# Kernel tuning notes

Measured on AMD Instinct MI355X. Metric: run time of the kernel, lower is better.

Reference implementation:

```python
import jax, jax.numpy as jnp
import numpy as np

IN_DIM = 32
OUT_DIM = 32
VAR_DIM = 64
BATCH = 16384
KER_DIMS = [1024, 1024, 1024, 1024]
NUM_STEPS = 8  # fixed-step RK4 stand-in for adaptive odeint (tol=1e-4)


def setup_inputs() -> dict:
    key = jax.random.key(0)
    ks = jax.random.split(key, 12)
    x = jax.random.normal(ks[0], (BATCH, IN_DIM), dtype=jnp.float32)
    aug = jnp.ones((BATCH, VAR_DIM - IN_DIM), dtype=jnp.float32)
    dims = [VAR_DIM] + KER_DIMS + [VAR_DIM]
    inp = {"x": x, "aug": aug}
    for i, (d1, d2) in enumerate(zip(dims[:-1], dims[1:])):
        # Linear(d1+1, d2): weight (d2, d1+1), bias (d2,)
        inp[f"W{i}"] = jax.random.normal(ks[1 + 2 * i], (d2, d1 + 1), dtype=jnp.float32) * 0.02
        inp[f"b{i}"] = jax.random.normal(ks[2 + 2 * i], (d2,), dtype=jnp.float32) * 0.02
    return inp


def _odefunc(t, y, Ws, bs):
    # y: [B, VAR_DIM]; per-layer concat of scalar time column, Linear, ReLU (except last)
    out = y
    n = len(Ws)
    for i, (W, b) in enumerate(zip(Ws, bs)):
        z = jnp.concatenate([out, jnp.full((out.shape[0], 1), t, dtype=out.dtype)], axis=1)
        out = z @ W.T + b
        if i < n - 1:
            out = jax.nn.relu(out)
    return out


def _integrate(y0, Ws, bs):
    dt = jnp.float32(1.0 / NUM_STEPS)

    def rk4_step(y, t):
        k1 = _odefunc(t, y, Ws, bs)
        k2 = _odefunc(t + 0.5 * dt, y + 0.5 * dt * k1, Ws, bs)
        k3 = _odefunc(t + 0.5 * dt, y + 0.5 * dt * k2, Ws, bs)
        k4 = _odefunc(t + dt, y + dt * k3, Ws, bs)
        return y + (dt / 6.0) * (k1 + 2.0 * k2 + 2.0 * k3 + k4), None

    ts = jnp.arange(NUM_STEPS, dtype=jnp.float32) * dt
    y1, _ = jax.lax.scan(rk4_step, y0, ts)
    return y1


def reference(x, aug, W0, b0, W1, b1, W2, b2, W3, b3, W4, b4):
    Ws = (W0, W1, W2, W3, W4)
    bs = (b0, b1, b2, b3, b4)
    y0 = jnp.concatenate([x, aug], axis=1)  # [B, VAR_DIM]
    y1 = _integrate(y0, Ws, bs)
    return y1[:, :OUT_DIM]
```

## Files before the change

kernel.cpp:

```cpp
#include <hip/hip_runtime.h>
#include <cstdint>
#include <cstddef>

#define BATCH 16384

typedef float f32x4 __attribute__((ext_vector_type(4)));
typedef _Float16 f16x8 __attribute__((ext_vector_type(8)));

__device__ __forceinline__ unsigned short f2h_bits(float f) {
  _Float16 h = (_Float16)f;
  return __builtin_bit_cast(unsigned short, h);
}

__device__ __forceinline__ void async_cp16(const void* g, void* l) {
  __builtin_amdgcn_global_load_lds(
      (const __attribute__((address_space(1))) unsigned int*)g,
      (__attribute__((address_space(3))) unsigned int*)l, 16, 0, 0);
}

#define PIPE_BAR_3() asm volatile("s_waitcnt vmcnt(3)\n\ts_barrier" ::: "memory")
#define PIPE_BAR_0() asm volatile("s_waitcnt vmcnt(0)\n\ts_barrier" ::: "memory")

template <int BM, int BN, int RT, int CT, int K, int N, bool RELU>
__launch_bounds__(512, 4)
__global__ void gemm_h(const unsigned short* __restrict__ A,
                       const unsigned short* __restrict__ Bw,
                       const float* __restrict__ Wfull,
                       const float* __restrict__ bias,
                       float tval,
                       unsigned short* __restrict__ Ch) {
  constexpr int BK = 32;
  constexpr int NI = K / BK;
  static_assert(NI >= 2, "pipeline needs >=2 stages");
  static_assert((BM * 4 + BN * 4) / 512 == 3, "vmcnt(3) assumes 3 loads/stage");
  static_assert(BM == 4 * RT * 16 && BN == 2 * CT * 16, "4x2 waves");
  __shared__ __align__(16) unsigned short smA[3][BM * BK];
  __shared__ __align__(16) unsigned short smB[3][BN * BK];
  __shared__ float biasLds[BN];

  const int tid = threadIdx.x;
  const int wave = tid >> 6;
  const int lane = tid & 63;
  const int quad = lane >> 4;
  const int r16 = lane & 15;

  const int rowA0 = blockIdx.x * BM;
  const int rowB0 = blockIdx.y * BN;
  const int waveM = wave >> 1;
  const int waveN = wave & 1;

  if (tid < BN) {
    const int col = rowB0 + tid;
    biasLds[tid] = bias[col] + tval * Wfull[(size_t)col * (K + 1) + K];
  }

  auto stage = [&](int k0, int buf) {
#pragma unroll
    for (int i = 0; i < BM * 4 / 512; ++i) {
      const int s = i * 512 + tid;
      const int row = s >> 2;
      const int c = (s & 3) ^ ((row >> 1) & 3);
      const unsigned short* g = A + (size_t)(rowA0 + row) * K + (k0 + c * 8);
      char* l = ((char*)smA[buf]) + (size_t)(i * 512 + (wave << 6)) * 16;
      async_cp16(g, l);
    }
    {
      const int s = tid;
      const int row = s >> 2;
      const int c = (s & 3) ^ ((row >> 1) & 3);
      const unsigned short* g = Bw + (size_t)(rowB0 + row) * K + (k0 + c * 8);
      char* l = ((char*)smB[buf]) + (size_t)((wave << 6)) * 16;
      async_cp16(g, l);
    }
  };

  f32x4 acc[RT][CT];
  const f32x4 zero = {0.f, 0.f, 0.f, 0.f};
#pragma unroll
  for (int i = 0; i < RT; ++i)
#pragma unroll
    for (int j = 0; j < CT; ++j) acc[i][j] = zero;

  auto compute = [&](int buf) {
    const unsigned short* sA = smA[buf];
    const unsigned short* sB = smB[buf];
    f16x8 af[RT], bfr[CT];
#pragma unroll
    for (int nt = 0; nt < CT; ++nt) {
      const int row = waveN * (CT * 16) + nt * 16 + r16;
      const int cp = quad ^ ((row >> 1) & 3);
      bfr[nt] = *(const f16x8*)(sB + row * BK + cp * 8);
    }
#pragma unroll
    for (int mt = 0; mt < RT; ++mt) {
      const int row = waveM * (RT * 16) + mt * 16 + r16;
      const int cp = quad ^ ((row >> 1) & 3);
      af[mt] = *(const f16x8*)(sA + row * BK + cp * 8);
    }
#pragma unroll
    for (int mt = 0; mt < RT; ++mt)
#pragma unroll
      for (int nt = 0; nt < CT; ++nt)
        acc[mt][nt] =
            __builtin_amdgcn_mfma_f32_16x16x32_f16(af[mt], bfr[nt], acc[mt][nt], 0, 0, 0);
  };

  stage(0, 0);
  stage(BK, 1);

#pragma unroll
  for (int kk = 0; kk < NI - 1; ++kk) {
    PIPE_BAR_3();
    if (kk + 2 < NI) stage((kk + 2) * BK, (kk + 2) % 3);
    compute(kk % 3);
  }
  PIPE_BAR_0();
  compute((NI - 1) % 3);

#pragma unroll
  for (int mt = 0; mt < RT; ++mt) {
    const int grow0 = rowA0 + waveM * (RT * 16) + mt * 16 + quad * 4;
#pragma unroll
    for (int nt = 0; nt < CT; ++nt) {
      const int lcol = waveN * (CT * 16) + nt * 16 + r16;
      const int gcol = rowB0 + lcol;
      const float bi = biasLds[lcol];
#pragma unroll
      for (int r = 0; r < 4; ++r) {
        float v = acc[mt][nt][r] + bi;
        if (RELU) v = fmaxf(v, 0.0f);
        Ch[(size_t)(grow0 + r) * N + gcol] = f2h_bits(v);
      }
    }
  }
}

__launch_bounds__(256, 4)
__global__ void gemm_l4(const unsigned short* __restrict__ A,
                        const unsigned short* __restrict__ Bw,
                        const float* __restrict__ Wfull,
                        const float* __restrict__ bias,
                        float tval,
                        float* __restrict__ y, float* __restrict__ ksum,
                        unsigned short* __restrict__ yh,
                        float* __restrict__ outp, int mode, float dt) {
  constexpr int K = 1024, BK = 32, BM = 32, BN = 64, NI = K / BK;
  __shared__ __align__(16) unsigned short smA[2][BM * BK];
  __shared__ __align__(16) unsigned short smB[2][BN * BK];
  __shared__ float biasLds[BN];

  const int tid = threadIdx.x;
  const int wave = tid >> 6;
  const int lane = tid & 63;
  const int quad = lane >> 4;
  const int r16 = lane & 15;

  const int rowA0 = blockIdx.x * BM;
  const int waveM = wave >> 1;
  const int waveN = wave & 1;

  if (tid < BN) {
    biasLds[tid] = bias[tid] + tval * Wfull[(size_t)tid * (K + 1) + K];
  }

  auto stage = [&](int k0, int buf) {
    if (tid < BM * 4) {
      const int s = tid;
      const int row = s >> 2;
      const int c = (s & 3) ^ ((row >> 1) & 3);
      const unsigned short* g = A + (size_t)(rowA0 + row) * K + (k0 + c * 8);
      char* l = ((char*)smA[buf]) + (size_t)(wave << 6) * 16;
      async_cp16(g, l);
    }
    {
      const int s = tid;
      const int row = s >> 2;
      const int c = (s & 3) ^ ((row >> 1) & 3);
      const unsigned short* g = Bw + (size_t)row * K + (k0 + c * 8);
      char* l = ((char*)smB[buf]) + (size_t)(wave << 6) * 16;
      async_cp16(g, l);
    }
  };

  f32x4 acc[2];
  const f32x4 zero = {0.f, 0.f, 0.f, 0.f};
  acc[0] = zero; acc[1] = zero;

  stage(0, 0);

#pragma unroll 2
  for (int kk = 0; kk < NI; ++kk) {
    __syncthreads();
    if (kk + 1 < NI) stage((kk + 1) * BK, (kk + 1) & 1);

    const unsigned short* sA = smA[kk & 1];
    const unsigned short* sB = smB[kk & 1];
    f16x8 af, bfr[2];
    {
      const int row = waveM * 16 + r16;
      const int cp = quad ^ ((row >> 1) & 3);
      af = *(const f16x8*)(sA + row * BK + cp * 8);
    }
#pragma unroll
    for (int nt = 0; nt < 2; ++nt) {
      const int row = (waveN * 2 + nt) * 16 + r16;
      const int cp = quad ^ ((row >> 1) & 3);
      bfr[nt] = *(const f16x8*)(sB + row * BK + cp * 8);
    }
#pragma unroll
    for (int nt = 0; nt < 2; ++nt)
      acc[nt] = __builtin_amdgcn_mfma_f32_16x16x32_f16(af, bfr[nt], acc[nt], 0, 0, 0);
  }

  const int grow0 = rowA0 + waveM * 16 + quad * 4;
#pragma unroll
  for (int nt = 0; nt < 2; ++nt) {
    const int col = waveN * 32 + nt * 16 + r16;
    const float bi = biasLds[col];
#pragma unroll
    for (int r = 0; r < 4; ++r) {
      const float k = acc[nt][r] + bi;
      const int row = grow0 + r;
      const int idx = row * 64 + col;
      if (mode == 0) {
        ksum[idx] = k;
        yh[idx] = f2h_bits(y[idx] + 0.5f * dt * k);
      } else if (mode == 1) {
        ksum[idx] += 2.f * k;
        yh[idx] = f2h_bits(y[idx] + 0.5f * dt * k);
      } else if (mode == 2) {
        ksum[idx] += 2.f * k;
        yh[idx] = f2h_bits(y[idx] + dt * k);
      } else {
        const float yn = y[idx] + (dt / 6.f) * (ksum[idx] + k);
        y[idx] = yn;
        yh[idx] = f2h_bits(yn);
        if (outp && col < 32) outp[row * 32 + col] = yn;
      }
    }
  }
}

__global__ void conv_w(const float* __restrict__ W, unsigned short* __restrict__ Wh,
                       int N, int K) {
  const int idx = blockIdx.x * 256 + threadIdx.x;
  if (idx < N * K) {
    const int n = idx / K;
    const int k = idx - n * K;
    Wh[idx] = f2h_bits(W[(size_t)n * (K + 1) + k]);
  }
}

__global__ void init_y(const float* __restrict__ x, const float* __restrict__ aug,
                       float* __restrict__ y, unsigned short* __restrict__ yh) {
  const int idx = blockIdx.x * 256 + threadIdx.x;
  const int i = idx >> 6;
  const int j = idx & 63;
  const float v = (j < 32) ? x[i * 32 + j] : aug[i * 32 + (j - 32)];
  y[idx] = v;
  yh[idx] = f2h_bits(v);
}

extern "C" void kernel_launch(void* const* d_in, const int* in_sizes, int n_in,
                              void* d_out, int out_size, void* d_ws, size_t ws_size,
                              hipStream_t stream) {
  const float* x = (const float*)d_in[0];
  const float* aug = (const float*)d_in[1];
  const float* W[5];
  const float* b[5];
  for (int i = 0; i < 5; ++i) {
    W[i] = (const float*)d_in[2 + 2 * i];
    b[i] = (const float*)d_in[3 + 2 * i];
  }

  char* ws = (char*)d_ws;
  auto alloc = [&](size_t bytes) -> char* {
    char* p = ws;
    ws += (bytes + 255) & ~(size_t)255;
    return p;
  };
  float* y = (float*)alloc((size_t)BATCH * 64 * 4);
  unsigned short* yh = (unsigned short*)alloc((size_t)BATCH * 64 * 2);
  unsigned short* h1 = (unsigned short*)alloc((size_t)BATCH * 1024 * 2);
  unsigned short* h2 = (unsigned short*)alloc((size_t)BATCH * 1024 * 2);
  float* ksum = (float*)alloc((size_t)BATCH * 64 * 4);
  const int Kdim[5] = {64, 1024, 1024, 1024, 1024};
  const int Ndim[5] = {1024, 1024, 1024, 1024, 64};
  unsigned short* Wh[5];
  for (int i = 0; i < 5; ++i)
    Wh[i] = (unsigned short*)alloc((size_t)Ndim[i] * Kdim[i] * 2);

  for (int i = 0; i < 5; ++i) {
    const int total = Ndim[i] * Kdim[i];
    conv_w<<<(total + 255) / 256, 256, 0, stream>>>(W[i], Wh[i], Ndim[i], Kdim[i]);
  }
  init_y<<<BATCH * 64 / 256, 256, 0, stream>>>(x, aug, y, yh);

  const float dt = 0.125f;
  float* outp = (float*)d_out;

  auto eval = [&](float t, int mode, float* op) {
    gemm_h<256, 128, 4, 4, 64, 1024, true>
        <<<dim3(BATCH / 256, 1024 / 128), 512, 0, stream>>>(
            yh, Wh[0], W[0], b[0], t, h1);
    unsigned short* src = h1;
    unsigned short* dst = h2;
    for (int L = 1; L <= 3; ++L) {
      gemm_h<256, 128, 4, 4, 1024, 1024, true>
          <<<dim3(BATCH / 256, 1024 / 128), 512, 0, stream>>>(
              src, Wh[L], W[L], b[L], t, dst);
      unsigned short* tmp = src; src = dst; dst = tmp;
    }
    gemm_l4<<<dim3(BATCH / 32, 1), 256, 0, stream>>>(
        src, Wh[4], W[4], b[4], t, y, ksum, yh, op, mode, dt);
  };

  for (int s = 0; s < 8; ++s) {
    const float t0 = s * dt;
    eval(t0, 0, nullptr);
    eval(t0 + 0.5f * dt, 1, nullptr);
    eval(t0 + 0.5f * dt, 2, nullptr);
    eval(t0 + dt, 3, (s == 7) ? outp : nullptr);
  }
}
```

Measured before the change: 4.499 ms.

## Add 256x256 pipelined GEMM kernel with phased LDS loads for hidden layers

Replaces the 256x128 tile GEMM used for the three 1024x1024 hidden layers with a new 256x256 tile kernel using BK=64, double-buffered async global-to-LDS staging split across four phases per tile, XOR-swizzled LDS, and setprio around the MFMA bursts. The larger tile raises arithmetic intensity per loaded byte, and interleaving staging with compute is meant to hide global load latency. It uses 128 KB of LDS and many accumulator registers, which limits occupancy, and the grid shrinks to 256 blocks.

```diff
diff --git a/kernel.cpp b/kernel.cpp
--- a/kernel.cpp
+++ b/kernel.cpp
@@ -130,6 +130,142 @@
         float v = acc[mt][nt][r] + bi;
         if (RELU) v = fmaxf(v, 0.0f);
         Ch[(size_t)(grow0 + r) * N + gcol] = f2h_bits(v);
+      }
+    }
+  }
+}
+
+#define SBAR  asm volatile("s_barrier" ::: "memory")
+#define MBAR  asm volatile("s_waitcnt lgkmcnt(0)\n\ts_barrier" ::: "memory")
+#define VBAR8 asm volatile("s_waitcnt vmcnt(8)\n\ts_barrier" ::: "memory")
+#define VBAR0 asm volatile("s_waitcnt vmcnt(0)\n\ts_barrier" ::: "memory")
+
+#define PHASE(sA_, sB_, Q, STAGE_STMT, BND)                                   \
+  {                                                                           \
+    if ((Q) == 0) {                                                           \
+      _Pragma("unroll") for (int nt = 0; nt < 4; ++nt) {                      \
+        const int row = wc * 64 + nt * 16 + r16;                              \
+        const int sw = row & 7;                                               \
+        const unsigned short* bp = (sB_) + row * 64;                          \
+        bfr[nt][0] = *(const f16x8*)(bp + ((quad ^ sw) << 3));                \
+        bfr[nt][1] = *(const f16x8*)(bp + (((4 + quad) ^ sw) << 3));          \
+      }                                                                       \
+    }                                                                         \
+    f16x8 af0[2], af1[2];                                                     \
+    _Pragma("unroll") for (int mi = 0; mi < 2; ++mi) {                        \
+      const int row = wr * 128 + ((Q) * 2 + mi) * 16 + r16;                   \
+      const int sw = row & 7;                                                 \
+      const unsigned short* ap = (sA_) + row * 64;                            \
+      af0[mi] = *(const f16x8*)(ap + ((quad ^ sw) << 3));                     \
+      af1[mi] = *(const f16x8*)(ap + (((4 + quad) ^ sw) << 3));               \
+    }                                                                         \
+    MBAR;                                                                     \
+    STAGE_STMT;                                                               \
+    __builtin_amdgcn_s_setprio(1);                                            \
+    _Pragma("unroll") for (int mi = 0; mi < 2; ++mi)                          \
+      _Pragma("unroll") for (int nt = 0; nt < 4; ++nt) {                      \
+        acc[(Q) * 2 + mi][nt] = __builtin_amdgcn_mfma_f32_16x16x32_f16(       \
+            af0[mi], bfr[nt][0], acc[(Q) * 2 + mi][nt], 0, 0, 0);             \
+        acc[(Q) * 2 + mi][nt] = __builtin_amdgcn_mfma_f32_16x16x32_f16(       \
+            af1[mi], bfr[nt][1], acc[(Q) * 2 + mi][nt], 0, 0, 0);             \
+      }                                                                       \
+    __builtin_amdgcn_s_setprio(0);                                            \
+    BND;                                                                      \
+  }
+
+#define TILE(sA_, sB_, STG0, STG1, STG3, BND)  \
+  {                                            \
+    f16x8 bfr[4][2];                           \
+    PHASE(sA_, sB_, 0, STG0, SBAR)             \
+    PHASE(sA_, sB_, 1, STG1, SBAR)             \
+    PHASE(sA_, sB_, 2, ;, SBAR)                \
+    PHASE(sA_, sB_, 3, STG3, BND)              \
+  }
+
+__launch_bounds__(512, 2)
+__global__ void gemm8(const unsigned short* __restrict__ A,
+                      const unsigned short* __restrict__ Bw,
+                      const float* __restrict__ Wfull,
+                      const float* __restrict__ bias,
+                      float tval,
+                      unsigned short* __restrict__ Ch) {
+  __shared__ __align__(16) unsigned short smA[2][256 * 64];
+  __shared__ __align__(16) unsigned short smB[2][256 * 64];
+  __shared__ float biasLds[256];
+
+  const int tid = threadIdx.x;
+  const int wave = tid >> 6;
+  const int lane = tid & 63;
+  const int quad = lane >> 4;
+  const int r16 = lane & 15;
+  const int wr = wave >> 2;
+  const int wc = wave & 3;
+
+  const int rowA0 = blockIdx.x * 256;
+  const int rowB0 = blockIdx.y * 256;
+  const unsigned short* Ag = A + (size_t)rowA0 * 1024;
+  const unsigned short* Bg = Bw + (size_t)rowB0 * 1024;
+
+  if (tid < 256) {
+    const int col = rowB0 + tid;
+    biasLds[tid] = bias[col] + tval * Wfull[(size_t)col * 1025 + 1024];
+  }
+
+  auto stg = [&](const unsigned short* gbase, unsigned short* lds, int k0, int half) {
+#pragma unroll
+    for (int i = 0; i < 2; ++i) {
+      const int s = half * 1024 + i * 512 + tid;
+      const int row = s >> 3;
+      const int c = (s & 7) ^ (row & 7);
+      const unsigned short* g = gbase + (size_t)row * 1024 + (k0 + (c << 3));
+      char* l = (char*)lds + (size_t)(half * 1024 + i * 512 + (wave << 6)) * 16;
+      async_cp16(g, l);
+    }
+  };
+
+  f32x4 acc[8][4];
+  const f32x4 zero = {0.f, 0.f, 0.f, 0.f};
+#pragma unroll
+  for (int i = 0; i < 8; ++i)
+#pragma unroll
+    for (int j = 0; j < 4; ++j) acc[i][j] = zero;
+
+  stg(Bg, smB[0], 0, 0);  stg(Bg, smB[0], 0, 1);
+  stg(Ag, smA[0], 0, 0);  stg(Ag, smA[0], 0, 1);
+  stg(Bg, smB[1], 64, 0); stg(Bg, smB[1], 64, 1);
+  stg(Ag, smA[1], 64, 0); stg(Ag, smA[1], 64, 1);
+  VBAR8;
+
+  for (int tt = 0; tt < 14; tt += 2) {
+    const int kn0 = (tt + 2) * 64;
+    const int kn1 = (tt + 3) * 64;
+    TILE(smA[0], smB[0],
+         stg(Bg, smB[0], kn0, 0),
+         stg(Bg, smB[0], kn0, 1),
+         (stg(Ag, smA[0], kn0, 0), stg(Ag, smA[0], kn0, 1)),
+         VBAR8)
+    TILE(smA[1], smB[1],
+         stg(Bg, smB[1], kn1, 0),
+         stg(Bg, smB[1], kn1, 1),
+         (stg(Ag, smA[1], kn1, 0), stg(Ag, smA[1], kn1, 1)),
+         VBAR8)
+  }
+  TILE(smA[0], smB[0], ;, ;, ;, VBAR0)
+  TILE(smA[1], smB[1], ;, ;, ;, ;)
+
+#pragma unroll
+  for (int mt = 0; mt < 8; ++mt) {
+    const int grow0 = rowA0 + wr * 128 + mt * 16 + quad * 4;
+#pragma unroll
+    for (int nt = 0; nt < 4; ++nt) {
+      const int lcol = wc * 64 + nt * 16 + r16;
+      const int gcol = rowB0 + lcol;
+      const float bi = biasLds[lcol];
+#pragma unroll
+      for (int r = 0; r < 4; ++r) {
+        float v = acc[mt][nt][r] + bi;
+        v = fmaxf(v, 0.0f);
+        Ch[(size_t)(grow0 + r) * 1024 + gcol] = f2h_bits(v);
       }
     }
   }
@@ -306,9 +442,8 @@
     unsigned short* src = h1;
     unsigned short* dst = h2;
     for (int L = 1; L <= 3; ++L) {
-      gemm_h<256, 128, 4, 4, 1024, 1024, true>
-          <<<dim3(BATCH / 256, 1024 / 128), 512, 0, stream>>>(
-              src, Wh[L], W[L], b[L], t, dst);
+      gemm8<<<dim3(BATCH / 256, 1024 / 256), 512, 0, stream>>>(
+          src, Wh[L], W[L], b[L], t, dst);
       unsigned short* tmp = src; src = dst; dst = tmp;
     }
     gemm_l4<<<dim3(BATCH / 32, 1), 256, 0, stream>>>(
```

After: 4.473 ms. About the same (-0.6%).

## Load hidden-layer weight fragments directly from global, staging only activations in LDS

Applied to the files above, without the earlier changes.

Adds a gemm_hb variant for the three 1024x1024 hidden layers. Only the activation tile goes through the async global-to-LDS triple buffer. Each wave reads its weight (B) fragments straight from global memory into registers every K step, and the pipeline wait is lowered to vmcnt(2). This cuts LDS traffic and shared-memory footprint and drops the B staging loads, but it exposes global/L2 load latency on the B fragments inside each iteration. Those fragments are also loaded redundantly by the four waves that share a column slice.

```diff
diff --git a/kernel.cpp b/kernel.cpp
--- a/kernel.cpp
+++ b/kernel.cpp
@@ -19,6 +19,7 @@
 }
 
 #define PIPE_BAR_3() asm volatile("s_waitcnt vmcnt(3)\n\ts_barrier" ::: "memory")
+#define PIPE_BAR_2() asm volatile("s_waitcnt vmcnt(2)\n\ts_barrier" ::: "memory")
 #define PIPE_BAR_0() asm volatile("s_waitcnt vmcnt(0)\n\ts_barrier" ::: "memory")
 
 template <int BM, int BN, int RT, int CT, int K, int N, bool RELU>
@@ -116,6 +117,109 @@
   }
   PIPE_BAR_0();
   compute((NI - 1) % 3);
+
+#pragma unroll
+  for (int mt = 0; mt < RT; ++mt) {
+    const int grow0 = rowA0 + waveM * (RT * 16) + mt * 16 + quad * 4;
+#pragma unroll
+    for (int nt = 0; nt < CT; ++nt) {
+      const int lcol = waveN * (CT * 16) + nt * 16 + r16;
+      const int gcol = rowB0 + lcol;
+      const float bi = biasLds[lcol];
+#pragma unroll
+      for (int r = 0; r < 4; ++r) {
+        float v = acc[mt][nt][r] + bi;
+        if (RELU) v = fmaxf(v, 0.0f);
+        Ch[(size_t)(grow0 + r) * N + gcol] = f2h_bits(v);
+      }
+    }
+  }
+}
+
+template <int BM, int BN, int RT, int CT, int K, int N, bool RELU>
+__launch_bounds__(512, 4)
+__global__ void gemm_hb(const unsigned short* __restrict__ A,
+                        const unsigned short* __restrict__ Bw,
+                        const float* __restrict__ Wfull,
+                        const float* __restrict__ bias,
+                        float tval,
+                        unsigned short* __restrict__ Ch) {
+  constexpr int BK = 32;
+  constexpr int NI = K / BK;
+  static_assert(NI >= 2, "pipeline needs >=2 stages");
+  static_assert(BM * 4 / 512 == 2, "A stage = 2 loads/thread");
+  static_assert(BM == 4 * RT * 16 && BN == 2 * CT * 16, "4x2 waves");
+  __shared__ __align__(16) unsigned short smA[3][BM * BK];
+  __shared__ float biasLds[BN];
+
+  const int tid = threadIdx.x;
+  const int wave = tid >> 6;
+  const int lane = tid & 63;
+  const int quad = lane >> 4;
+  const int r16 = lane & 15;
+
+  const int rowA0 = blockIdx.x * BM;
+  const int rowB0 = blockIdx.y * BN;
+  const int waveM = wave >> 1;
+  const int waveN = wave & 1;
+
+  if (tid < BN) {
+    const int col = rowB0 + tid;
+    biasLds[tid] = bias[col] + tval * Wfull[(size_t)col * (K + 1) + K];
+  }
+
+  auto stage = [&](int k0, int buf) {
+#pragma unroll
+    for (int i = 0; i < 2; ++i) {
+      const int s = i * 512 + tid;
+      const int row = s >> 2;
+      const int c = (s & 3) ^ ((row >> 1) & 3);
+      const unsigned short* g = A + (size_t)(rowA0 + row) * K + (k0 + c * 8);
+      char* l = ((char*)smA[buf]) + (size_t)(i * 512 + (wave << 6)) * 16;
+      async_cp16(g, l);
+    }
+  };
+
+  f32x4 acc[RT][CT];
+  const f32x4 zero = {0.f, 0.f, 0.f, 0.f};
+#pragma unroll
+  for (int i = 0; i < RT; ++i)
+#pragma unroll
+    for (int j = 0; j < CT; ++j) acc[i][j] = zero;
+
+  stage(0, 0);
+  stage(BK, 1);
+
+#pragma unroll
+  for (int kk = 0; kk < NI; ++kk) {
+    PIPE_BAR_2();
+
+    f16x8 bfr[CT];
+#pragma unroll
+    for (int nt = 0; nt < CT; ++nt) {
+      const int row = rowB0 + waveN * (CT * 16) + nt * 16 + r16;
+      bfr[nt] = *(const f16x8*)(Bw + (size_t)row * K + kk * BK + quad * 8);
+    }
+    __builtin_amdgcn_sched_barrier(0);
+
+    if (kk + 2 < NI) stage((kk + 2) * BK, (kk + 2) % 3);
+    __builtin_amdgcn_sched_barrier(0);
+
+    const unsigned short* sA = smA[kk % 3];
+    f16x8 af[RT];
+#pragma unroll
+    for (int mt = 0; mt < RT; ++mt) {
+      const int row = waveM * (RT * 16) + mt * 16 + r16;
+      const int cp = quad ^ ((row >> 1) & 3);
+      af[mt] = *(const f16x8*)(sA + row * BK + cp * 8);
+    }
+#pragma unroll
+    for (int mt = 0; mt < RT; ++mt)
+#pragma unroll
+      for (int nt = 0; nt < CT; ++nt)
+        acc[mt][nt] =
+            __builtin_amdgcn_mfma_f32_16x16x32_f16(af[mt], bfr[nt], acc[mt][nt], 0, 0, 0);
+  }
 
 #pragma unroll
   for (int mt = 0; mt < RT; ++mt) {
@@ -306,7 +410,7 @@
     unsigned short* src = h1;
     unsigned short* dst = h2;
     for (int L = 1; L <= 3; ++L) {
-      gemm_h<256, 128, 4, 4, 1024, 1024, true>
+      gemm_hb<256, 128, 4, 4, 1024, 1024, true>
           <<<dim3(BATCH / 256, 1024 / 128), 512, 0, stream>>>(
               src, Wh[L], W[L], b[L], t, dst);
       unsigned short* tmp = src; src = dst; dst = tmp;
```

Result: slower. 8.327 ms (+85.1%).
